# Kernel optimization log

Measured on AMD Instinct MI355X. Metric: run time of the kernel, lower is better.

The kernel has to match this reference:

```python
import jax, jax.numpy as jnp
import numpy as np

N, D = 8192, 1024


def setup_inputs() -> dict:
    key = jax.random.key(0)
    k1, k2 = jax.random.split(key)
    x = jax.random.normal(k1, (N, D), dtype=jnp.float32)
    # scale weight like a trained linear layer (~1/sqrt(D)) so softmax isn't fully saturated
    W = jax.random.normal(k2, (D, D), dtype=jnp.float32) * (1.0 / np.sqrt(D))
    b = jnp.zeros((D,), dtype=jnp.float32)
    recency_weight = jnp.full((1,), -0.5, dtype=jnp.float32)  # nn.Parameter init in source
    return {"x": x, "W": W, "b": b, "recency_weight": recency_weight}


def reference(x, W, b, recency_weight):
    # linear + relu
    x_proj = jax.nn.relu(x @ W.T + b)          # [N, D]
    # tied self-matmul
    scores = x_proj @ x_proj.T                  # [N, N]
    n = x.shape[0]
    idx = jnp.arange(n)
    # causal mask: upper triangle strictly above diagonal (use_current_timestep=True)
    upper = idx[None, :] > idx[:, None]         # [N, N] bool
    scores = jnp.where(upper, -jnp.inf, scores)
    # recency bias: toeplitz |i - j|, zeroed on masked (upper) part, scaled by recency_weight
    dist = jnp.abs(idx[:, None] - idx[None, :]).astype(scores.dtype)
    recency = recency_weight[0] * jnp.where(upper, 0.0, dist)
    scores = scores + recency
    return jax.nn.softmax(scores, axis=1)       # [N, N] lower-triangular attention
```

## Files before the change

### kernel.cpp

```cpp
#include <hip/hip_runtime.h>
#include <hip/hip_fp8.h>
#include <math.h>

#define NR 8192
#define DIM 1024
#define BK 32

#if __has_builtin(__builtin_amdgcn_cvt_pk_fp8_f32) && __has_builtin(__builtin_amdgcn_cvt_f32_fp8)
#define HW_FP8 1
#else
#define HW_FP8 0
#endif

typedef __attribute__((ext_vector_type(4))) float f32x4;
typedef __attribute__((ext_vector_type(4))) int   i32x4;

static __device__ __forceinline__ unsigned char f2fp8(float f) {
  __hip_fp8_e4m3 q(f);
  return *reinterpret_cast<const unsigned char*>(&q);
}

static __device__ __forceinline__ float fp82f(unsigned char c) {
  __hip_fp8_e4m3 h;
  h.__x = (__hip_fp8_storage_t)c;
  return (float)h;
}

static __device__ __forceinline__ void gload_lds16(const void* g, void* lds) {
  __builtin_amdgcn_global_load_lds(
      (const __attribute__((address_space(1))) unsigned int*)g,
      (__attribute__((address_space(3))) unsigned int*)lds, 16, 0, 0);
}

__global__ __launch_bounds__(256) void zerok(float* __restrict__ p, int n) {
  int i = blockIdx.x * 256 + threadIdx.x;
  if (i < n) p[i] = 0.0f;
}

__global__ __launch_bounds__(256) void cvt_fp8(const float* __restrict__ in,
                                               unsigned char* __restrict__ outp,
                                               int n8) {
  int i = blockIdx.x * 256 + threadIdx.x;
  if (i < n8) {
    float4 a = ((const float4*)in)[2 * i];
    float4 b = ((const float4*)in)[2 * i + 1];
#if HW_FP8
    unsigned int w1 = 0, w2 = 0;
    w1 = __builtin_amdgcn_cvt_pk_fp8_f32(a.x, a.y, w1, false);
    w1 = __builtin_amdgcn_cvt_pk_fp8_f32(a.z, a.w, w1, true);
    w2 = __builtin_amdgcn_cvt_pk_fp8_f32(b.x, b.y, w2, false);
    w2 = __builtin_amdgcn_cvt_pk_fp8_f32(b.z, b.w, w2, true);
    uint2 o; o.x = w1; o.y = w2;
    ((uint2*)outp)[i] = o;
#else
    union { unsigned char c[8]; uint2 u; } o;
    o.c[0] = f2fp8(a.x); o.c[1] = f2fp8(a.y); o.c[2] = f2fp8(a.z); o.c[3] = f2fp8(a.w);
    o.c[4] = f2fp8(b.x); o.c[5] = f2fp8(b.y); o.c[6] = f2fp8(b.z); o.c[7] = f2fp8(b.w);
    ((uint2*)outp)[i] = o.u;
#endif
  }
}

static __device__ __forceinline__ void gemm_core_fp8(const unsigned char* A,
                                                     const unsigned char* B,
                                                     int m0, int n0,
                                                     unsigned char* S,
                                                     f32x4 acc[4][4]) {
  const int tid  = threadIdx.x;
  const int lane = tid & 63;
  const int wave = tid >> 6;
  const int wr = wave >> 1, wc = wave & 1;
  const int li = lane & 15, g = lane >> 4;
  const int ar  = wave * 32 + (lane >> 1);
  const int acl = (lane & 1) ^ ((ar >> 2) & 1);
  const int pc = ((g >> 1) ^ ((li >> 2) & 1)) * 16 + (g & 1) * 8;

#define ISSUE_TILE8(t_)                                                             \
  do {                                                                              \
    const int kt_ = (t_) * BK;                                                      \
    unsigned char* buf_ = S + ((t_) & 3) * 8192;                                    \
    gload_lds16(A + (size_t)(m0 + ar) * DIM + kt_ + acl * 16,                       \
                buf_ + wave * 1024);                                                \
    gload_lds16(B + (size_t)(n0 + ar) * DIM + kt_ + acl * 16,                       \
                buf_ + 4096 + wave * 1024);                                         \
  } while (0)

  ISSUE_TILE8(0);
  ISSUE_TILE8(1);
  ISSUE_TILE8(2);

  for (int t = 0; t < DIM / BK; ++t) {
    if (t <= DIM / BK - 3)      asm volatile("s_waitcnt vmcnt(4)" ::: "memory");
    else if (t == DIM / BK - 2) asm volatile("s_waitcnt vmcnt(2)" ::: "memory");
    else                        asm volatile("s_waitcnt vmcnt(0)" ::: "memory");
    __builtin_amdgcn_s_barrier();

    const unsigned char* Ab = S + (t & 3) * 8192;
    const unsigned char* Bb = Ab + 4096;
    long av[4], bv[4];
#pragma unroll
    for (int m = 0; m < 4; ++m)
      av[m] = *(const long*)(Ab + (wr * 64 + m * 16 + li) * 32 + pc);
#pragma unroll
    for (int n = 0; n < 4; ++n)
      bv[n] = *(const long*)(Bb + (wc * 64 + n * 16 + li) * 32 + pc);
    asm volatile("s_waitcnt lgkmcnt(0)" ::: "memory");
    if (t + 3 < DIM / BK) ISSUE_TILE8(t + 3);
#pragma unroll
    for (int m = 0; m < 4; ++m)
#pragma unroll
      for (int n = 0; n < 4; ++n)
        acc[m][n] = __builtin_amdgcn_mfma_f32_16x16x32_fp8_fp8(av[m], bv[n], acc[m][n], 0, 0, 0);
  }
#undef ISSUE_TILE8
}

static __device__ __forceinline__ void gemm_core_i8(const signed char* A,
                                                    const signed char* B,
                                                    int m0, int n0,
                                                    signed char* S,
                                                    i32x4 acc[4][4]) {
  const int tid  = threadIdx.x;
  const int lane = tid & 63;
  const int wave = tid >> 6;
  const int wr = wave >> 1, wc = wave & 1;
  const int li = lane & 15, g = lane >> 4;
  const int tr = tid >> 2;
  const int c  = (tid & 3) ^ ((tr >> 1) & 3);
  const int pco = (g ^ ((li >> 1) & 3)) * 16;

#define ISSUE_I8(t_)                                                                \
  do {                                                                              \
    const int kt_ = (t_) * 64;                                                      \
    signed char* buf_ = S + ((t_) % 3) * 16384;                                     \
    gload_lds16(A + (size_t)(m0 + tr)      * DIM + kt_ + c * 16,                    \
                buf_ + wave * 1024);                                                \
    gload_lds16(A + (size_t)(m0 + 64 + tr) * DIM + kt_ + c * 16,                    \
                buf_ + 4096 + wave * 1024);                                         \
    gload_lds16(B + (size_t)(n0 + tr)      * DIM + kt_ + c * 16,                    \
                buf_ + 8192 + wave * 1024);                                         \
    gload_lds16(B + (size_t)(n0 + 64 + tr) * DIM + kt_ + c * 16,                    \
                buf_ + 12288 + wave * 1024);                                        \
  } while (0)

  ISSUE_I8(0);
  ISSUE_I8(1);
  ISSUE_I8(2);

  const int NT = DIM / 64;
  for (int t = 0; t < NT; ++t) {
    if (t <= NT - 3)      asm volatile("s_waitcnt vmcnt(8)" ::: "memory");
    else if (t == NT - 2) asm volatile("s_waitcnt vmcnt(4)" ::: "memory");
    else                  asm volatile("s_waitcnt vmcnt(0)" ::: "memory");
    __builtin_amdgcn_s_barrier();

    const signed char* Ab = S + (t % 3) * 16384;
    const signed char* Bb = Ab + 8192;
    i32x4 av[4], bv[4];
#pragma unroll
    for (int m = 0; m < 4; ++m)
      av[m] = *(const i32x4*)(Ab + (wr * 64 + m * 16 + li) * 64 + pco);
#pragma unroll
    for (int n = 0; n < 4; ++n)
      bv[n] = *(const i32x4*)(Bb + (wc * 64 + n * 16 + li) * 64 + pco);
    asm volatile("s_waitcnt lgkmcnt(0)" ::: "memory");
    if (t + 3 < NT) ISSUE_I8(t + 3);
#pragma unroll
    for (int m = 0; m < 4; ++m)
#pragma unroll
      for (int n = 0; n < 4; ++n)
        acc[m][n] = __builtin_amdgcn_mfma_i32_16x16x64_i8(av[m], bv[n], acc[m][n], 0, 0, 0);
  }
#undef ISSUE_I8
}

__global__ __launch_bounds__(256) void gemm1_relu(const unsigned char* __restrict__ Xq,
                                                  const unsigned char* __restrict__ Wq,
                                                  const float* __restrict__ bias,
                                                  signed char* __restrict__ XPi,
                                                  float* __restrict__ diag) {
  __shared__ unsigned char S[32768];
  const int m0 = blockIdx.y * 128, n0 = blockIdx.x * 128;
  f32x4 acc[4][4] = {};
  gemm_core_fp8(Xq, Wq, m0, n0, S, acc);

  const int lane = threadIdx.x & 63, wave = threadIdx.x >> 6;
  const int wr = wave >> 1, wc = wave & 1, g = lane >> 4, li = lane & 15;
  float bv[4];
#pragma unroll
  for (int n = 0; n < 4; ++n) bv[n] = bias[n0 + wc * 64 + n * 16 + li];
#pragma unroll
  for (int m = 0; m < 4; ++m) {
#pragma unroll
    for (int r = 0; r < 4; ++r) {
      int row = m0 + wr * 64 + m * 16 + g * 4 + r;
      float ds = 0.0f;
#pragma unroll
      for (int n = 0; n < 4; ++n) {
        int col = n0 + wc * 64 + n * 16 + li;
        float v = fmaxf(acc[m][n][r] + bv[n], 0.0f);
        int qv = __float2int_rn(v * 32.0f);
        qv = min(qv, 127);
        XPi[(size_t)row * DIM + col] = (signed char)qv;
        float vq = (float)qv * (1.0f / 32.0f);
        ds += vq * vq;
      }
#pragma unroll
      for (int off = 1; off < 16; off <<= 1) ds += __shfl_xor(ds, off);
      if (li == 0) atomicAdd(&diag[row], ds);
    }
  }
}

__global__ __launch_bounds__(256) void gemm2_scores(const signed char* __restrict__ XPi,
                                                    const float* __restrict__ rwp,
                                                    unsigned char* __restrict__ P8,
                                                    const float* __restrict__ diag,
                                                    float* __restrict__ Lrow) {
  int t = ((int)blockIdx.x & 7) * 260 + ((int)blockIdx.x >> 3);
  int by = (int)((sqrtf(8.0f * (float)t + 1.0f) - 1.0f) * 0.5f);
  while ((by + 1) * (by + 2) / 2 <= t) ++by;
  while (by * (by + 1) / 2 > t) --by;
  const int bx = t - by * (by + 1) / 2;

  __shared__ signed char S[49152];
  const int m0 = by * 128, n0 = bx * 128;
  i32x4 acc[4][4] = {};
  gemm_core_i8(XPi, XPi, m0, n0, S, acc);

  const float rw = rwp[0];
  const float qs = 1.0f / 1024.0f;
  const int lane = threadIdx.x & 63, wave = threadIdx.x >> 6;
  const int wr = wave >> 1, wc = wave & 1, g = lane >> 4, li = lane & 15;

#pragma unroll
  for (int m = 0; m < 4; ++m) {
#pragma unroll
    for (int r = 0; r < 4; ++r) {
      const int row = m0 + wr * 64 + m * 16 + g * 4 + r;
      const float dg = diag[row];
      float e[4];
#pragma unroll
      for (int n = 0; n < 4; ++n) {
        int col = n0 + wc * 64 + n * 16 + li;
        float v = (float)acc[m][n][r] * qs;
        v = (col <= row) ? v + rw * (float)(row - col) : -INFINITY;
        e[n] = __expf(v - dg);
      }
      float se;
#if HW_FP8
      unsigned int w = 0;
      w = __builtin_amdgcn_cvt_pk_fp8_f32(e[0], e[1], w, false);
      w = __builtin_amdgcn_cvt_pk_fp8_f32(e[2], e[3], w, true);
      se = __builtin_amdgcn_cvt_f32_fp8(w, 0) + __builtin_amdgcn_cvt_f32_fp8(w, 1) +
           __builtin_amdgcn_cvt_f32_fp8(w, 2) + __builtin_amdgcn_cvt_f32_fp8(w, 3);
#pragma unroll
      for (int n = 0; n < 4; ++n) {
        int col = n0 + wc * 64 + n * 16 + li;
        if (col <= row) P8[(size_t)row * NR + col] = (unsigned char)(w >> (8 * n));
      }
#else
      se = 0.0f;
#pragma unroll
      for (int n = 0; n < 4; ++n) {
        int col = n0 + wc * 64 + n * 16 + li;
        unsigned char eb = f2fp8(e[n]);
        se += fp82f(eb);
        if (col <= row) P8[(size_t)row * NR + col] = eb;
      }
#endif
#pragma unroll
      for (int off = 1; off < 16; off <<= 1) se += __shfl_xor(se, off);
      if (li == 0) atomicAdd(&Lrow[row], se);
    }
  }
}

__global__ __launch_bounds__(256) void normk(const unsigned char* __restrict__ P8,
                                             float* __restrict__ out,
                                             const float* __restrict__ Lrow) {
  const size_t idx = (size_t)blockIdx.x * 256 + threadIdx.x;
  const int row = (int)(idx >> 11);
  const int j0 = (int)(idx & 2047) * 4;
  f32x4* p = (f32x4*)out + idx;
  if (j0 > row) {
    f32x4 z = {0.f, 0.f, 0.f, 0.f};
    __builtin_nontemporal_store(z, p);
    return;
  }
  const float sc = __builtin_amdgcn_rcpf(Lrow[row]);
  unsigned int qw = *(const unsigned int*)(P8 + (size_t)row * NR + j0);
  f32x4 o;
#if HW_FP8
  o.x = __builtin_amdgcn_cvt_f32_fp8(qw, 0) * sc;
  o.y = __builtin_amdgcn_cvt_f32_fp8(qw, 1) * sc;
  o.z = __builtin_amdgcn_cvt_f32_fp8(qw, 2) * sc;
  o.w = __builtin_amdgcn_cvt_f32_fp8(qw, 3) * sc;
#else
  o.x = fp82f((unsigned char)(qw      )) * sc;
  o.y = fp82f((unsigned char)(qw >>  8)) * sc;
  o.z = fp82f((unsigned char)(qw >> 16)) * sc;
  o.w = fp82f((unsigned char)(qw >> 24)) * sc;
#endif
  if (j0 + 3 > row) {
    if (j0 + 1 > row) o.y = 0.f;
    if (j0 + 2 > row) o.z = 0.f;
    o.w = 0.f;
  }
  __builtin_nontemporal_store(o, p);
}

extern "C" void kernel_launch(void* const* d_in, const int* in_sizes, int n_in,
                              void* d_out, int out_size, void* d_ws, size_t ws_size,
                              hipStream_t stream) {
  const float* x  = (const float*)d_in[0];
  const float* W  = (const float*)d_in[1];
  const float* b  = (const float*)d_in[2];
  const float* rw = (const float*)d_in[3];
  float* out = (float*)d_out;

  char* ws = (char*)d_ws;
  unsigned char* Xq  = (unsigned char*)(ws);
  unsigned char* Wq  = (unsigned char*)(ws + (size_t)(8 << 20));
  signed char*   XPi = (signed char*)(ws + (size_t)(18 << 20));
  float* diag = (float*)(ws + (size_t)(34 << 20));
  float* Lrow = (float*)(ws + (size_t)(34 << 20) + 32768);
  unsigned char* P8 = (unsigned char*)(ws + (size_t)(64 << 20));

  zerok<<<(2 * NR + 255) / 256, 256, 0, stream>>>(diag, 2 * NR);
  cvt_fp8<<<NR * DIM / 8 / 256, 256, 0, stream>>>(x, Xq, NR * DIM / 8);
  cvt_fp8<<<DIM * DIM / 8 / 256, 256, 0, stream>>>(W, Wq, DIM * DIM / 8);
  gemm1_relu<<<dim3(DIM / 128, NR / 128), 256, 0, stream>>>(Xq, Wq, b, XPi, diag);
  gemm2_scores<<<2080, 256, 0, stream>>>(XPi, rw, P8, diag, Lrow);
  normk<<<(NR / 4) * (NR / 256), 256, 0, stream>>>(P8, out, Lrow);
}
```

Measured before the change: 406.0 us.

## Switch first GEMM to int8 MFMA, fuse zeroing into convert, widen normalize kernel

```diff
diff --git a/kernel.cpp b/kernel.cpp
--- a/kernel.cpp
+++ b/kernel.cpp
@@ -4,7 +4,6 @@
 
 #define NR 8192
 #define DIM 1024
-#define BK 32
 
 #if __has_builtin(__builtin_amdgcn_cvt_pk_fp8_f32) && __has_builtin(__builtin_amdgcn_cvt_f32_fp8)
 #define HW_FP8 1
@@ -32,87 +31,25 @@
       (__attribute__((address_space(3))) unsigned int*)lds, 16, 0, 0);
 }
 
-__global__ __launch_bounds__(256) void zerok(float* __restrict__ p, int n) {
+__global__ __launch_bounds__(256) void cvt_i8(const float* __restrict__ in,
+                                              signed char* __restrict__ outp,
+                                              float scale, int n8,
+                                              float* __restrict__ zbuf, int nz) {
   int i = blockIdx.x * 256 + threadIdx.x;
-  if (i < n) p[i] = 0.0f;
-}
-
-__global__ __launch_bounds__(256) void cvt_fp8(const float* __restrict__ in,
-                                               unsigned char* __restrict__ outp,
-                                               int n8) {
-  int i = blockIdx.x * 256 + threadIdx.x;
+  if (i < nz) zbuf[i] = 0.0f;
   if (i < n8) {
     float4 a = ((const float4*)in)[2 * i];
     float4 b = ((const float4*)in)[2 * i + 1];
-#if HW_FP8
-    unsigned int w1 = 0, w2 = 0;
-    w1 = __builtin_amdgcn_cvt_pk_fp8_f32(a.x, a.y, w1, false);
-    w1 = __builtin_amdgcn_cvt_pk_fp8_f32(a.z, a.w, w1, true);
-    w2 = __builtin_amdgcn_cvt_pk_fp8_f32(b.x, b.y, w2, false);
-    w2 = __builtin_amdgcn_cvt_pk_fp8_f32(b.z, b.w, w2, true);
-    uint2 o; o.x = w1; o.y = w2;
-    ((uint2*)outp)[i] = o;
-#else
-    union { unsigned char c[8]; uint2 u; } o;
-    o.c[0] = f2fp8(a.x); o.c[1] = f2fp8(a.y); o.c[2] = f2fp8(a.z); o.c[3] = f2fp8(a.w);
-    o.c[4] = f2fp8(b.x); o.c[5] = f2fp8(b.y); o.c[6] = f2fp8(b.z); o.c[7] = f2fp8(b.w);
+    float v[8] = {a.x, a.y, a.z, a.w, b.x, b.y, b.z, b.w};
+    union { signed char c[8]; uint2 u; } o;
+#pragma unroll
+    for (int k = 0; k < 8; ++k) {
+      int q = __float2int_rn(v[k] * scale);
+      q = max(min(q, 127), -127);
+      o.c[k] = (signed char)q;
+    }
     ((uint2*)outp)[i] = o.u;
-#endif
-  }
-}
-
-static __device__ __forceinline__ void gemm_core_fp8(const unsigned char* A,
-                                                     const unsigned char* B,
-                                                     int m0, int n0,
-                                                     unsigned char* S,
-                                                     f32x4 acc[4][4]) {
-  const int tid  = threadIdx.x;
-  const int lane = tid & 63;
-  const int wave = tid >> 6;
-  const int wr = wave >> 1, wc = wave & 1;
-  const int li = lane & 15, g = lane >> 4;
-  const int ar  = wave * 32 + (lane >> 1);
-  const int acl = (lane & 1) ^ ((ar >> 2) & 1);
-  const int pc = ((g >> 1) ^ ((li >> 2) & 1)) * 16 + (g & 1) * 8;
-
-#define ISSUE_TILE8(t_)                                                             \
-  do {                                                                              \
-    const int kt_ = (t_) * BK;                                                      \
-    unsigned char* buf_ = S + ((t_) & 3) * 8192;                                    \
-    gload_lds16(A + (size_t)(m0 + ar) * DIM + kt_ + acl * 16,                       \
-                buf_ + wave * 1024);                                                \
-    gload_lds16(B + (size_t)(n0 + ar) * DIM + kt_ + acl * 16,                       \
-                buf_ + 4096 + wave * 1024);                                         \
-  } while (0)
-
-  ISSUE_TILE8(0);
-  ISSUE_TILE8(1);
-  ISSUE_TILE8(2);
-
-  for (int t = 0; t < DIM / BK; ++t) {
-    if (t <= DIM / BK - 3)      asm volatile("s_waitcnt vmcnt(4)" ::: "memory");
-    else if (t == DIM / BK - 2) asm volatile("s_waitcnt vmcnt(2)" ::: "memory");
-    else                        asm volatile("s_waitcnt vmcnt(0)" ::: "memory");
-    __builtin_amdgcn_s_barrier();
-
-    const unsigned char* Ab = S + (t & 3) * 8192;
-    const unsigned char* Bb = Ab + 4096;
-    long av[4], bv[4];
-#pragma unroll
-    for (int m = 0; m < 4; ++m)
-      av[m] = *(const long*)(Ab + (wr * 64 + m * 16 + li) * 32 + pc);
-#pragma unroll
-    for (int n = 0; n < 4; ++n)
-      bv[n] = *(const long*)(Bb + (wc * 64 + n * 16 + li) * 32 + pc);
-    asm volatile("s_waitcnt lgkmcnt(0)" ::: "memory");
-    if (t + 3 < DIM / BK) ISSUE_TILE8(t + 3);
-#pragma unroll
-    for (int m = 0; m < 4; ++m)
-#pragma unroll
-      for (int n = 0; n < 4; ++n)
-        acc[m][n] = __builtin_amdgcn_mfma_f32_16x16x32_fp8_fp8(av[m], bv[n], acc[m][n], 0, 0, 0);
-  }
-#undef ISSUE_TILE8
+  }
 }
 
 static __device__ __forceinline__ void gemm_core_i8(const signed char* A,
@@ -174,16 +111,17 @@
 #undef ISSUE_I8
 }
 
-__global__ __launch_bounds__(256) void gemm1_relu(const unsigned char* __restrict__ Xq,
-                                                  const unsigned char* __restrict__ Wq,
+__global__ __launch_bounds__(256) void gemm1_relu(const signed char* __restrict__ Xi,
+                                                  const signed char* __restrict__ Wi,
                                                   const float* __restrict__ bias,
                                                   signed char* __restrict__ XPi,
                                                   float* __restrict__ diag) {
-  __shared__ unsigned char S[32768];
+  __shared__ signed char S[49152];
   const int m0 = blockIdx.y * 128, n0 = blockIdx.x * 128;
-  f32x4 acc[4][4] = {};
-  gemm_core_fp8(Xq, Wq, m0, n0, S, acc);
-
+  i32x4 acc[4][4] = {};
+  gemm_core_i8(Xi, Wi, m0, n0, S, acc);
+
+  const float qs1 = 1.0f / 16384.0f;
   const int lane = threadIdx.x & 63, wave = threadIdx.x >> 6;
   const int wr = wave >> 1, wc = wave & 1, g = lane >> 4, li = lane & 15;
   float bv[4];
@@ -198,7 +136,7 @@
 #pragma unroll
       for (int n = 0; n < 4; ++n) {
         int col = n0 + wc * 64 + n * 16 + li;
-        float v = fmaxf(acc[m][n][r] + bv[n], 0.0f);
+        float v = fmaxf((float)acc[m][n][r] * qs1 + bv[n], 0.0f);
         int qv = __float2int_rn(v * 32.0f);
         qv = min(qv, 127);
         XPi[(size_t)row * DIM + col] = (signed char)qv;
@@ -279,35 +217,39 @@
 __global__ __launch_bounds__(256) void normk(const unsigned char* __restrict__ P8,
                                              float* __restrict__ out,
                                              const float* __restrict__ Lrow) {
-  const size_t idx = (size_t)blockIdx.x * 256 + threadIdx.x;
-  const int row = (int)(idx >> 11);
-  const int j0 = (int)(idx & 2047) * 4;
-  f32x4* p = (f32x4*)out + idx;
-  if (j0 > row) {
-    f32x4 z = {0.f, 0.f, 0.f, 0.f};
-    __builtin_nontemporal_store(z, p);
-    return;
-  }
-  const float sc = __builtin_amdgcn_rcpf(Lrow[row]);
-  unsigned int qw = *(const unsigned int*)(P8 + (size_t)row * NR + j0);
-  f32x4 o;
+  const size_t base = (size_t)blockIdx.x * 512 + threadIdx.x;
+#pragma unroll
+  for (int k = 0; k < 2; ++k) {
+    const size_t idx = base + k * 256;
+    const int row = (int)(idx >> 11);
+    const int j0 = (int)(idx & 2047) * 4;
+    f32x4* p = (f32x4*)out + idx;
+    if (j0 > row) {
+      f32x4 z = {0.f, 0.f, 0.f, 0.f};
+      __builtin_nontemporal_store(z, p);
+      continue;
+    }
+    const float sc = __builtin_amdgcn_rcpf(Lrow[row]);
+    unsigned int qw = *(const unsigned int*)(P8 + (size_t)row * NR + j0);
+    f32x4 o;
 #if HW_FP8
-  o.x = __builtin_amdgcn_cvt_f32_fp8(qw, 0) * sc;
-  o.y = __builtin_amdgcn_cvt_f32_fp8(qw, 1) * sc;
-  o.z = __builtin_amdgcn_cvt_f32_fp8(qw, 2) * sc;
-  o.w = __builtin_amdgcn_cvt_f32_fp8(qw, 3) * sc;
+    o.x = __builtin_amdgcn_cvt_f32_fp8(qw, 0) * sc;
+    o.y = __builtin_amdgcn_cvt_f32_fp8(qw, 1) * sc;
+    o.z = __builtin_amdgcn_cvt_f32_fp8(qw, 2) * sc;
+    o.w = __builtin_amdgcn_cvt_f32_fp8(qw, 3) * sc;
 #else
-  o.x = fp82f((unsigned char)(qw      )) * sc;
-  o.y = fp82f((unsigned char)(qw >>  8)) * sc;
-  o.z = fp82f((unsigned char)(qw >> 16)) * sc;
-  o.w = fp82f((unsigned char)(qw >> 24)) * sc;
+    o.x = fp82f((unsigned char)(qw      )) * sc;
+    o.y = fp82f((unsigned char)(qw >>  8)) * sc;
+    o.z = fp82f((unsigned char)(qw >> 16)) * sc;
+    o.w = fp82f((unsigned char)(qw >> 24)) * sc;
 #endif
-  if (j0 + 3 > row) {
-    if (j0 + 1 > row) o.y = 0.f;
-    if (j0 + 2 > row) o.z = 0.f;
-    o.w = 0.f;
-  }
-  __builtin_nontemporal_store(o, p);
+    if (j0 + 3 > row) {
+      if (j0 + 1 > row) o.y = 0.f;
+      if (j0 + 2 > row) o.z = 0.f;
+      o.w = 0.f;
+    }
+    __builtin_nontemporal_store(o, p);
+  }
 }
 
 extern "C" void kernel_launch(void* const* d_in, const int* in_sizes, int n_in,
@@ -320,17 +262,18 @@
   float* out = (float*)d_out;
 
   char* ws = (char*)d_ws;
-  unsigned char* Xq  = (unsigned char*)(ws);
-  unsigned char* Wq  = (unsigned char*)(ws + (size_t)(8 << 20));
-  signed char*   XPi = (signed char*)(ws + (size_t)(18 << 20));
+  signed char* Xi  = (signed char*)(ws);
+  signed char* Wi  = (signed char*)(ws + (size_t)(8 << 20));
+  signed char* XPi = (signed char*)(ws + (size_t)(18 << 20));
   float* diag = (float*)(ws + (size_t)(34 << 20));
   float* Lrow = (float*)(ws + (size_t)(34 << 20) + 32768);
   unsigned char* P8 = (unsigned char*)(ws + (size_t)(64 << 20));
 
-  zerok<<<(2 * NR + 255) / 256, 256, 0, stream>>>(diag, 2 * NR);
-  cvt_fp8<<<NR * DIM / 8 / 256, 256, 0, stream>>>(x, Xq, NR * DIM / 8);
-  cvt_fp8<<<DIM * DIM / 8 / 256, 256, 0, stream>>>(W, Wq, DIM * DIM / 8);
-  gemm1_relu<<<dim3(DIM / 128, NR / 128), 256, 0, stream>>>(Xq, Wq, b, XPi, diag);
+  cvt_i8<<<NR * DIM / 8 / 256, 256, 0, stream>>>(x, Xi, 32.0f, NR * DIM / 8,
+                                                 diag, 2 * NR);
+  cvt_i8<<<DIM * DIM / 8 / 256, 256, 0, stream>>>(W, Wi, 512.0f, DIM * DIM / 8,
+                                                  (float*)nullptr, 0);
+  gemm1_relu<<<dim3(DIM / 128, NR / 128), 256, 0, stream>>>(Xi, Wi, b, XPi, diag);
   gemm2_scores<<<2080, 256, 0, stream>>>(XPi, rw, P8, diag, Lrow);
-  normk<<<(NR / 4) * (NR / 256), 256, 0, stream>>>(P8, out, Lrow);
-}
+  normk<<<NR / 4 * (NR / 256) / 2, 256, 0, stream>>>(P8, out, Lrow);
+}
```

After: 397.4 us. 1.02x faster.
